# Kernel tuning notes

Hardware: AMD Instinct MI355X
Metric: run time of the kernel (lower is better)

The kernel has to match this reference:

```python
import jax, jax.numpy as jnp
import numpy as np

B, S, D, H = 1, 2048, 1024, 16
HD = D // H  # head_dim = 64
ROPE_BASE = 10000.0


def _rope_cos_sin(seqlen, head_dim, dtype):
    inv_freq = 1.0 / (ROPE_BASE ** (jnp.arange(0, head_dim, 2, dtype=jnp.float32) / head_dim))
    t = jnp.arange(seqlen, dtype=jnp.float32)
    freqs = jnp.outer(t, inv_freq)                      # [S, HD/2]
    emb = jnp.concatenate([freqs, freqs], axis=-1)      # [S, HD]
    # broadcast shape [1, S, 1, HD] over (batch, seq, heads, head_dim)
    return jnp.cos(emb)[None, :, None, :].astype(dtype), jnp.sin(emb)[None, :, None, :].astype(dtype)


def _rotate_half(x):
    x1, x2 = jnp.split(x, 2, axis=-1)
    return jnp.concatenate([-x2, x1], axis=-1)


def setup_inputs() -> dict:
    key = jax.random.key(0)
    k1, k2, k3 = jax.random.split(key, 3)
    std_in = 1.0 / np.sqrt(D)
    std_out = std_in / np.sqrt(2.0)  # layer_id = 0
    x = jax.random.normal(k1, (B, S, D), dtype=jnp.float32)
    w_in = jax.random.normal(k2, (3 * H * HD, D), dtype=jnp.float32) * std_in
    w_out = jax.random.normal(k3, (D, H * HD), dtype=jnp.float32) * std_out
    return {"x": x, "w_in": w_in, "w_out": w_out, "is_causal": 1}


def reference(x, w_in, w_out, is_causal):
    b, s, _ = x.shape
    qkv = jnp.einsum('bsd,ed->bse', x, w_in)            # [B,S,3*H*HD]
    xq, xk, xv = jnp.split(qkv, 3, axis=-1)
    xq = xq.reshape(b, s, H, HD)
    xk = xk.reshape(b, s, H, HD)
    xv = xv.reshape(b, s, H, HD)
    cos, sin = _rope_cos_sin(s, HD, xq.dtype)
    xq = xq * cos + _rotate_half(xq) * sin
    xk = xk * cos + _rotate_half(xk) * sin
    scale = 1.0 / np.sqrt(HD)
    scores = jnp.einsum('bqhd,bkhd->bhqk', xq, xk) * scale  # [B,H,S,S]
    if is_causal:
        mask = jnp.tril(jnp.ones((s, s), dtype=bool))
        scores = jnp.where(mask[None, None], scores, jnp.finfo(scores.dtype).min)
    probs = jax.nn.softmax(scores, axis=-1)
    out = jnp.einsum('bhqk,bkhd->bqhd', probs, xv)      # [B,S,H,HD]
    out = out.reshape(b, s, H * HD)
    return jnp.einsum('bse,de->bsd', out, w_out)
```

## Files before the change

kernel.cpp:

```cpp
#include <hip/hip_runtime.h>
#include <stdint.h>

#define S_LEN 2048
#define DMODEL 1024
#define NHEAD 16
#define HDIM 64
#define NE 3072
#define C2 0.18033688011112042f
#define RINV (-13.287712379549449f / 32.f)

typedef __attribute__((ext_vector_type(8))) short short8_t;
typedef __attribute__((ext_vector_type(4))) float f32x4;
typedef __attribute__((ext_vector_type(16))) float f32x16;

__device__ __forceinline__ float bf2f(ushort u) {
  union { float f; uint32_t i; } c; c.i = ((uint32_t)u) << 16; return c.f;
}
__device__ __forceinline__ ushort f2bf(float f) {
  union { float f; uint32_t i; } c; c.f = f;
  uint32_t x = c.i;
  return (ushort)((x + 0x7fffu + ((x >> 16) & 1u)) >> 16);
}

__device__ __forceinline__ void gload_lds16(const ushort* g, ushort* l) {
  __builtin_amdgcn_global_load_lds(
      (const __attribute__((address_space(1))) void*)g,
      (__attribute__((address_space(3))) void*)l, 16, 0, 0);
}

__global__ void cvt_all(const float* __restrict__ x, const float* __restrict__ w_in,
                        const float* __restrict__ w_out,
                        ushort* __restrict__ xbf, ushort* __restrict__ winbf,
                        ushort* __restrict__ woutbf) {
  int i = blockIdx.x * blockDim.x + threadIdx.x;
  const float* src; ushort* dst; int off;
  if (i < 524288)       { src = x;     dst = xbf;    off = i; }
  else if (i < 1310720) { src = w_in;  dst = winbf;  off = i - 524288; }
  else                  { src = w_out; dst = woutbf; off = i - 1310720; }
  float4 v = ((const float4*)src)[off];
  ushort4 o;
  o.x = f2bf(v.x); o.y = f2bf(v.y); o.z = f2bf(v.z); o.w = f2bf(v.w);
  ((ushort4*)dst)[off] = o;
}

template<int BM, int BN, int BK, int MODE>
__global__ __launch_bounds__(256) void gemm_abt(
    const ushort* __restrict__ A, const ushort* __restrict__ B,
    void* __restrict__ Cv, ushort* __restrict__ kfrag, ushort* __restrict__ vfrag,
    int M, int N, int K)
{
  constexpr int AR = BM / 32;
  constexpr int AC = BN / 32;
  constexpr int NB = BK / 8;
  constexpr int RPC = 512 / BK;
  constexpr int NCH = (BM + BN) / RPC;
  constexpr int PG = NCH / 4;
  constexpr int KK = BK / 32;
  __shared__ ushort lds[(BM + BN) * BK];

  const int nbn = N / BN;
  const int bid = blockIdx.x;
  int bm, bn;
  if constexpr (MODE == 2) {
    int xcd = bid & 7, local = bid >> 3;
    int cc = local / 24, ii = local % 24;
    bm = 2 * xcd + ii / 12;
    bn = cc * 12 + ii % 12;
  } else {
    const int cpx = gridDim.x >> 3;
    int swz = (bid & 7) * cpx + (bid >> 3);
    bm = swz / nbn;
    bn = swz - bm * nbn;
  }
  const int tid = threadIdx.x;
  const int w = tid >> 6, l = tid & 63;
  const int wm = w >> 1, wn = w & 1;
  const int fr = l & 15, fg = l >> 4;

  f32x4 acc[AR][AC];
#pragma unroll
  for (int r = 0; r < AR; ++r)
#pragma unroll
    for (int c = 0; c < AC; ++c) acc[r][c] = (f32x4){0.f, 0.f, 0.f, 0.f};

  const ushort* gsrc[PG];
  ushort* ldst[PG];
#pragma unroll
  for (int i = 0; i < PG; ++i) {
    int ch = w + 4 * i;
    int row = ch * RPC + l / NB;
    int cb = (l % NB) ^ (row & (NB - 1));
    if (row < BM)
      gsrc[i] = A + (size_t)(bm * BM + row) * K + cb * 8;
    else
      gsrc[i] = B + (size_t)(bn * BN + (row - BM)) * K + cb * 8;
    ldst[i] = &lds[ch * 512];
  }

  const int sw = fr & (NB - 1);
  const int rowa = wm * (BM / 2) + fr;
  const int rowb = wn * (BN / 2) + fr;

  for (int k0 = 0; k0 < K; k0 += BK) {
    __syncthreads();
#pragma unroll
    for (int i = 0; i < PG; ++i) gload_lds16(gsrc[i] + k0, ldst[i]);
    __syncthreads();

#pragma unroll
    for (int kk = 0; kk < KK; ++kk) {
      short8_t af[AR], bfr[AC];
#pragma unroll
      for (int r = 0; r < AR; ++r) {
        union { short8_t v; uint4 q; } u;
        u.q = *(const uint4*)&lds[(rowa + r * 16) * BK + ((fg + 4 * kk) ^ sw) * 8];
        af[r] = u.v;
      }
#pragma unroll
      for (int c = 0; c < AC; ++c) {
        union { short8_t v; uint4 q; } u;
        u.q = *(const uint4*)&lds[BM * BK + (rowb + c * 16) * BK + ((fg + 4 * kk) ^ sw) * 8];
        bfr[c] = u.v;
      }
      __builtin_amdgcn_s_setprio(1);
#pragma unroll
      for (int r = 0; r < AR; ++r)
#pragma unroll
        for (int c = 0; c < AC; ++c)
          acc[r][c] = __builtin_amdgcn_mfma_f32_16x16x32_bf16(af[r], bfr[c], acc[r][c], 0, 0, 0);
      __builtin_amdgcn_s_setprio(0);
    }
  }

  if constexpr (MODE == 0) {
    const int row0 = bm * BM + wm * (BM / 2) + fg * 4;
    const int col0 = bn * BN + wn * (BN / 2) + fr;
#pragma unroll
    for (int r = 0; r < AR; ++r)
#pragma unroll
      for (int c = 0; c < AC; ++c)
#pragma unroll
        for (int j = 0; j < 4; ++j)
          ((float*)Cv)[(size_t)(row0 + r * 16 + j) * N + col0 + c * 16] = acc[r][c][j];
  } else {
    const int cls = bn >> 4;
    const int h = bn & 15;
    if (cls == 0) {
      const int row0 = bm * BM + wm * (BM / 2) + fg * 4;
      const int colq = bn * 64 + wn * 32 + fr;
      ushort* qb = (ushort*)Cv;
#pragma unroll
      for (int r = 0; r < AR; ++r)
#pragma unroll
        for (int c = 0; c < AC; ++c)
#pragma unroll
          for (int j = 0; j < 4; ++j)
            qb[(size_t)(row0 + r * 16 + j) * 1024 + colq + c * 16] = f2bf(acc[r][c][j]);
    } else {
      __syncthreads();
      ushort* T = lds;
#pragma unroll
      for (int r = 0; r < AR; ++r)
#pragma unroll
        for (int c = 0; c < AC; ++c)
#pragma unroll
          for (int j = 0; j < 4; ++j) {
            int rl = wm * 64 + r * 16 + fg * 4 + j;
            int cl = wn * 32 + c * 16 + fr;
            T[rl * 72 + cl] = f2bf(acc[r][c][j]);
          }
      __syncthreads();

      if (cls == 1) {
        const int ii = tid & 31;
        const float invf = exp2f((float)ii * RINV);
#pragma unroll
        for (int kk = 0; kk < 16; ++kk) {
          int key = (tid >> 5) * 16 + kk;
          float sn, cs;
          sincosf((float)(bm * 128 + key) * invf, &sn, &cs);
          float x1 = bf2f(T[key * 72 + ii]), x2 = bf2f(T[key * 72 + ii + 32]);
          T[key * 72 + ii]      = f2bf(x1 * cs - x2 * sn);
          T[key * 72 + ii + 32] = f2bf(x2 * cs + x1 * sn);
        }
        __syncthreads();
#pragma unroll
        for (int it = 0; it < 4; ++it) {
          int idx = tid + 256 * it;
          int tt = idx >> 9, e = idx & 511;
          int c2 = e >> 6, l2 = e & 63, q2 = l2 & 31, hi2 = l2 >> 5;
          int kh = c2 >> 2, ks = c2 & 3;
          uint4 v = *(const uint4*)&T[(64 * tt + 32 * kh + q2) * 72 + 16 * ks + 8 * hi2];
          *(uint4*)(kfrag + (size_t)(h * 32 + bm * 2 + tt) * 4096 + e * 8) = v;
        }
      } else {
#pragma unroll
        for (int it = 0; it < 4; ++it) {
          int idx = tid + 256 * it;
          int tt = idx >> 9, e = idx & 511;
          int c2 = e >> 6, l2 = e & 63, q2 = l2 & 31, hi2 = l2 >> 5;
          int ks = c2 >> 1, dh = c2 & 1;
          ushort tmp[8];
#pragma unroll
          for (int jj = 0; jj < 8; ++jj)
            tmp[jj] = T[(64 * tt + 16 * ks + 8 * hi2 + jj) * 72 + 32 * dh + q2];
          *(uint4*)(vfrag + (size_t)(h * 32 + bm * 2 + tt) * 4096 + e * 8) = *(const uint4*)tmp;
        }
      }
    }
  }
}

__global__ __launch_bounds__(256) void attn_mfma(
    const ushort* __restrict__ qbuf, const ushort* __restrict__ kfrag,
    const ushort* __restrict__ vfrag, ushort* __restrict__ O,
    const int* __restrict__ icausal)
{
  __shared__ ushort obf[4][32][68];
  __shared__ float mdl[4][32];

  const int bid = blockIdx.x;
  const int h = (bid & 7) * 2 + ((bid >> 3) & 1);
  const int i = bid >> 4;
  const int g = i & 15, k = i >> 4;
  const int qt = (k == 0) ? g : (k == 1) ? (63 - g) : (k == 2) ? (31 - g) : (32 + g);

  const int causal = *icausal;
  const int nt = causal ? ((qt >> 1) + 1) : (S_LEN / 64);

  const int tid = threadIdx.x;
  const int w = tid >> 6, l = tid & 63;
  const int q = l & 31, hi = l >> 5;
  const int q0 = qt * 32;
  const int qa = q0 + q;
  const int t0 = w * nt / 4, t1 = (w + 1) * nt / 4;

  short8_t qf[4];
  {
    const ushort* qp = qbuf + (size_t)qa * 1024 + h * HDIM + 8 * hi;
#pragma unroll
    for (int ks = 0; ks < 4; ++ks) {
      union { short8_t v; uint4 u; } uu;
      uu.u = *(const uint4*)(qp + 16 * ks);
      qf[ks] = uu.v;
    }
    union { short8_t v; ushort u[8]; } a0, a1, b0, b1;
    a0.v = qf[0]; a1.v = qf[1]; b0.v = qf[2]; b1.v = qf[3];
#pragma unroll
    for (int j = 0; j < 8; ++j) {
      {
        float invf = exp2f((float)(8 * hi + j) * RINV);
        float sn, cs; sincosf((float)qa * invf, &sn, &cs);
        float x1 = bf2f(a0.u[j]), x2 = bf2f(b0.u[j]);
        a0.u[j] = f2bf((x1 * cs - x2 * sn) * C2);
        b0.u[j] = f2bf((x2 * cs + x1 * sn) * C2);
      }
      {
        float invf = exp2f((float)(16 + 8 * hi + j) * RINV);
        float sn, cs; sincosf((float)qa * invf, &sn, &cs);
        float x1 = bf2f(a1.u[j]), x2 = bf2f(b1.u[j]);
        a1.u[j] = f2bf((x1 * cs - x2 * sn) * C2);
        b1.u[j] = f2bf((x2 * cs + x1 * sn) * C2);
      }
    }
    qf[0] = a0.v; qf[1] = a1.v; qf[2] = b0.v; qf[3] = b1.v;
  }

  const ushort* kb = kfrag + (size_t)(h * 32 + t0) * 4096 + l * 8;
  const ushort* vb = vfrag + (size_t)(h * 32 + t0) * 4096 + l * 8;

  float den = 0.f;
  f32x16 oacc[2];
#pragma unroll
  for (int d = 0; d < 2; ++d)
#pragma unroll
    for (int r = 0; r < 16; ++r) oacc[d][r] = 0.f;

  if (t0 < t1) {
    uint4 kq[8];
#pragma unroll
    for (int ks = 0; ks < 4; ++ks)
#pragma unroll
      for (int kh = 0; kh < 2; ++kh)
        kq[ks * 2 + kh] = *(const uint4*)(kb + (kh * 4 + ks) * 512);
    kb += 4096;

    for (int t = t0; t < t1; ++t) {
      uint4 vq[8];
#pragma unroll
      for (int c = 0; c < 8; ++c)
        vq[c] = *(const uint4*)(vb + c * 512);
      vb += 4096;

      f32x16 sacc[2];
#pragma unroll
      for (int kh = 0; kh < 2; ++kh)
#pragma unroll
        for (int r = 0; r < 16; ++r) sacc[kh][r] = 0.f;
      __builtin_amdgcn_s_setprio(1);
#pragma unroll
      for (int ks = 0; ks < 4; ++ks)
#pragma unroll
        for (int kh = 0; kh < 2; ++kh) {
          union { short8_t v; uint4 u; } ku;
          ku.u = kq[ks * 2 + kh];
          sacc[kh] = __builtin_amdgcn_mfma_f32_32x32x16_bf16(ku.v, qf[ks], sacc[kh], 0, 0, 0);
        }
      __builtin_amdgcn_s_setprio(0);

      if (t + 1 < t1) {
#pragma unroll
        for (int ks = 0; ks < 4; ++ks)
#pragma unroll
          for (int kh = 0; kh < 2; ++kh)
            kq[ks * 2 + kh] = *(const uint4*)(kb + (kh * 4 + ks) * 512);
        kb += 4096;
      }

      if (causal && t == nt - 1) {
        const int k0 = t * 64;
#pragma unroll
        for (int kh = 0; kh < 2; ++kh)
#pragma unroll
          for (int r = 0; r < 16; ++r)
            if (k0 + 32 * kh + (r & 3) + 8 * (r >> 2) + 4 * hi > qa) sacc[kh][r] = -3e38f;
      }

      float p0 = 0.f, p1 = 0.f, p2 = 0.f, p3 = 0.f;
      short8_t pa[4];
#pragma unroll
      for (int ks = 0; ks < 4; ++ks) {
        const int blk = ks >> 1, kp = (ks & 1) * 8;
        float e0 = exp2f(sacc[blk][kp + 0]);
        float e1 = exp2f(sacc[blk][kp + 1]);
        float e2 = exp2f(sacc[blk][kp + 2]);
        float e3 = exp2f(sacc[blk][kp + 3]);
        float e4 = exp2f(sacc[blk][kp + 4]);
        float e5 = exp2f(sacc[blk][kp + 5]);
        float e6 = exp2f(sacc[blk][kp + 6]);
        float e7 = exp2f(sacc[blk][kp + 7]);
        p0 += e0 + e4; p1 += e1 + e5; p2 += e2 + e6; p3 += e3 + e7;
        uint wL0, wL1, wH0, wH1;
        asm("v_cvt_pk_bf16_f32 %0, %1, %2" : "=v"(wL0) : "v"(e0), "v"(e1));
        asm("v_cvt_pk_bf16_f32 %0, %1, %2" : "=v"(wL1) : "v"(e2), "v"(e3));
        asm("v_cvt_pk_bf16_f32 %0, %1, %2" : "=v"(wH0) : "v"(e4), "v"(e5));
        asm("v_cvt_pk_bf16_f32 %0, %1, %2" : "=v"(wH1) : "v"(e6), "v"(e7));
        uint s0 = hi ? wL0 : wH0, s1 = hi ? wL1 : wH1;
        uint r0 = __shfl_xor(s0, 32), r1 = __shfl_xor(s1, 32);
        union { short8_t v; uint u[4]; } pu;
        pu.u[0] = hi ? r0 : wL0;
        pu.u[1] = hi ? r1 : wL1;
        pu.u[2] = hi ? wH0 : r0;
        pu.u[3] = hi ? wH1 : r1;
        pa[ks] = pu.v;
      }
      float psum = (p0 + p1) + (p2 + p3);
      psum += __shfl_xor(psum, 32);
      den += psum;

      __builtin_amdgcn_s_setprio(1);
#pragma unroll
      for (int ks = 0; ks < 4; ++ks)
#pragma unroll
        for (int dh = 0; dh < 2; ++dh) {
          union { short8_t v; uint4 u; } vu;
          vu.u = vq[ks * 2 + dh];
          oacc[dh] = __builtin_amdgcn_mfma_f32_32x32x16_bf16(vu.v, pa[ks], oacc[dh], 0, 0, 0);
        }
      __builtin_amdgcn_s_setprio(0);
    }
  }

#pragma unroll
  for (int dh = 0; dh < 2; ++dh)
#pragma unroll
    for (int rq = 0; rq < 4; ++rq) {
      uint a0, a1;
      asm("v_cvt_pk_bf16_f32 %0, %1, %2" : "=v"(a0) : "v"(oacc[dh][4 * rq + 0]), "v"(oacc[dh][4 * rq + 1]));
      asm("v_cvt_pk_bf16_f32 %0, %1, %2" : "=v"(a1) : "v"(oacc[dh][4 * rq + 2]), "v"(oacc[dh][4 * rq + 3]));
      uint2 dd; dd.x = a0; dd.y = a1;
      *(uint2*)&obf[w][q][32 * dh + 8 * rq + 4 * hi] = dd;
    }
  if (hi == 0) mdl[w][q] = den;
  __syncthreads();

  {
    const int qq = tid >> 3, d8 = tid & 7;
    float dt = mdl[0][qq] + mdl[1][qq] + mdl[2][qq] + mdl[3][qq];
    float inv = 1.f / dt;
    uint4 a = *(const uint4*)&obf[0][qq][d8 * 8];
    uint4 b = *(const uint4*)&obf[1][qq][d8 * 8];
    uint4 c = *(const uint4*)&obf[2][qq][d8 * 8];
    uint4 d = *(const uint4*)&obf[3][qq][d8 * 8];
    const ushort* ap = (const ushort*)&a;
    const ushort* bp = (const ushort*)&b;
    const ushort* cp = (const ushort*)&c;
    const ushort* dp = (const ushort*)&d;
    ushort out8[8];
#pragma unroll
    for (int e = 0; e < 8; ++e) {
      float acc = (bf2f(ap[e]) + bf2f(bp[e])) + (bf2f(cp[e]) + bf2f(dp[e]));
      out8[e] = f2bf(acc * inv);
    }
    *(uint4*)(O + (size_t)(q0 + qq) * DMODEL + h * HDIM + d8 * 8) = *(const uint4*)out8;
  }
}

extern "C" void kernel_launch(void* const* d_in, const int* in_sizes, int n_in,
                              void* d_out, int out_size, void* d_ws, size_t ws_size,
                              hipStream_t stream) {
  const float* x     = (const float*)d_in[0];
  const float* w_in  = (const float*)d_in[1];
  const float* w_out = (const float*)d_in[2];
  const int* icausal = (const int*)d_in[3];

  char* ws = (char*)d_ws;
  ushort* xbf    = (ushort*)(ws);
  ushort* winbf  = (ushort*)(ws + 4194304);
  ushort* woutbf = (ushort*)(ws + 10485760);
  ushort* qbuf   = (ushort*)(ws + 12582912);
  ushort* kfrag  = (ushort*)(ws + 16777216);
  ushort* vfrag  = (ushort*)(ws + 20971520);
  ushort* obuf   = (ushort*)(ws + 25165824);

  cvt_all<<<6144, 256, 0, stream>>>(x, w_in, w_out, xbf, winbf, woutbf);

  gemm_abt<128, 64, 128, 2><<<16 * 48, 256, 0, stream>>>(xbf, winbf, (void*)qbuf, kfrag, vfrag, 2048, 3072, 1024);
  attn_mfma<<<1024, 256, 0, stream>>>(qbuf, kfrag, vfrag, obuf, icausal);
  gemm_abt<64, 64, 128, 0><<<32 * 16, 256, 0, stream>>>(obuf, woutbf, d_out, nullptr, nullptr, 2048, 1024, 1024);
}
```

Before: 72.74 us.

## Fuse fp32-to-bf16 conversion into GEMM tile loads and drop the conversion kernel

Removes the standalone kernel that converted x, w_in and w_out to bf16. The GEMMs now read fp32 operands directly, convert them in registers with packed bf16 conversion instructions, and store the result into the swizzled LDS tile. The bf16 attention output still uses the async global-to-LDS path. This removes a kernel launch and a full write-then-reread round trip of the converted data. In exchange, the GEMM inner loop fetches twice the bytes per operand, converts shared weight tiles redundantly in every block, and replaces async LDS loads with synchronous loads routed through registers.

```diff
diff --git a/kernel.cpp b/kernel.cpp
--- a/kernel.cpp
+++ b/kernel.cpp
@@ -28,24 +28,9 @@
       (__attribute__((address_space(3))) void*)l, 16, 0, 0);
 }
 
-__global__ void cvt_all(const float* __restrict__ x, const float* __restrict__ w_in,
-                        const float* __restrict__ w_out,
-                        ushort* __restrict__ xbf, ushort* __restrict__ winbf,
-                        ushort* __restrict__ woutbf) {
-  int i = blockIdx.x * blockDim.x + threadIdx.x;
-  const float* src; ushort* dst; int off;
-  if (i < 524288)       { src = x;     dst = xbf;    off = i; }
-  else if (i < 1310720) { src = w_in;  dst = winbf;  off = i - 524288; }
-  else                  { src = w_out; dst = woutbf; off = i - 1310720; }
-  float4 v = ((const float4*)src)[off];
-  ushort4 o;
-  o.x = f2bf(v.x); o.y = f2bf(v.y); o.z = f2bf(v.z); o.w = f2bf(v.w);
-  ((ushort4*)dst)[off] = o;
-}
-
 template<int BM, int BN, int BK, int MODE>
 __global__ __launch_bounds__(256) void gemm_abt(
-    const ushort* __restrict__ A, const ushort* __restrict__ B,
+    const void* __restrict__ Av, const float* __restrict__ Bf,
     void* __restrict__ Cv, ushort* __restrict__ kfrag, ushort* __restrict__ vfrag,
     int M, int N, int K)
 {
@@ -83,18 +68,30 @@
 #pragma unroll
     for (int c = 0; c < AC; ++c) acc[r][c] = (f32x4){0.f, 0.f, 0.f, 0.f};
 
-  const ushort* gsrc[PG];
-  ushort* ldst[PG];
-#pragma unroll
-  for (int i = 0; i < PG; ++i) {
-    int ch = w + 4 * i;
-    int row = ch * RPC + l / NB;
-    int cb = (l % NB) ^ (row & (NB - 1));
-    if (row < BM)
-      gsrc[i] = A + (size_t)(bm * BM + row) * K + cb * 8;
-    else
-      gsrc[i] = B + (size_t)(bn * BN + (row - BM)) * K + cb * 8;
-    ldst[i] = &lds[ch * 512];
+  const char* gp[PG];
+  ushort* ldp[PG];
+  bool ia[PG];
+  {
+    const int lrow = l / NB, cb = l % NB;
+#pragma unroll
+    for (int i = 0; i < PG; ++i) {
+      int ch = w + 4 * i;
+      int row = ch * RPC + lrow;
+      int scb = cb ^ (row & (NB - 1));
+      ia[i] = (ch * RPC) < BM;
+      if (ia[i]) {
+        if constexpr (MODE == 0) {
+          gp[i] = (const char*)((const ushort*)Av + (size_t)(bm * BM + row) * K + scb * 8);
+          ldp[i] = &lds[ch * 512];
+        } else {
+          gp[i] = (const char*)((const float*)Av + (size_t)(bm * BM + row) * K + cb * 8);
+          ldp[i] = &lds[ch * 512 + lrow * BK + scb * 8];
+        }
+      } else {
+        gp[i] = (const char*)(Bf + (size_t)(bn * BN + (row - BM)) * K + cb * 8);
+        ldp[i] = &lds[ch * 512 + lrow * BK + scb * 8];
+      }
+    }
   }
 
   const int sw = fr & (NB - 1);
@@ -104,7 +101,22 @@
   for (int k0 = 0; k0 < K; k0 += BK) {
     __syncthreads();
 #pragma unroll
-    for (int i = 0; i < PG; ++i) gload_lds16(gsrc[i] + k0, ldst[i]);
+    for (int i = 0; i < PG; ++i) {
+      if (MODE == 0 && ia[i]) {
+        gload_lds16((const ushort*)gp[i] + k0, ldp[i]);
+      } else {
+        const float* s = (const float*)gp[i] + k0;
+        float4 f0 = *(const float4*)s;
+        float4 f1 = *(const float4*)(s + 4);
+        uint u0, u1, u2, u3;
+        asm("v_cvt_pk_bf16_f32 %0, %1, %2" : "=v"(u0) : "v"(f0.x), "v"(f0.y));
+        asm("v_cvt_pk_bf16_f32 %0, %1, %2" : "=v"(u1) : "v"(f0.z), "v"(f0.w));
+        asm("v_cvt_pk_bf16_f32 %0, %1, %2" : "=v"(u2) : "v"(f1.x), "v"(f1.y));
+        asm("v_cvt_pk_bf16_f32 %0, %1, %2" : "=v"(u3) : "v"(f1.z), "v"(f1.w));
+        uint4 uu; uu.x = u0; uu.y = u1; uu.z = u2; uu.w = u3;
+        *(uint4*)ldp[i] = uu;
+      }
+    }
     __syncthreads();
 
 #pragma unroll
@@ -415,17 +427,14 @@
   const int* icausal = (const int*)d_in[3];
 
   char* ws = (char*)d_ws;
-  ushort* xbf    = (ushort*)(ws);
-  ushort* winbf  = (ushort*)(ws + 4194304);
-  ushort* woutbf = (ushort*)(ws + 10485760);
   ushort* qbuf   = (ushort*)(ws + 12582912);
   ushort* kfrag  = (ushort*)(ws + 16777216);
   ushort* vfrag  = (ushort*)(ws + 20971520);
   ushort* obuf   = (ushort*)(ws + 25165824);
 
-  cvt_all<<<6144, 256, 0, stream>>>(x, w_in, w_out, xbf, winbf, woutbf);
-
-  gemm_abt<128, 64, 128, 2><<<16 * 48, 256, 0, stream>>>(xbf, winbf, (void*)qbuf, kfrag, vfrag, 2048, 3072, 1024);
+  gemm_abt<128, 64, 128, 2><<<16 * 48, 256, 0, stream>>>(
+      (const void*)x, w_in, (void*)qbuf, kfrag, vfrag, 2048, 3072, 1024);
   attn_mfma<<<1024, 256, 0, stream>>>(qbuf, kfrag, vfrag, obuf, icausal);
-  gemm_abt<64, 64, 128, 0><<<32 * 16, 256, 0, stream>>>(obuf, woutbf, d_out, nullptr, nullptr, 2048, 1024, 1024);
-}
+  gemm_abt<64, 64, 128, 0><<<32 * 16, 256, 0, stream>>>(
+      (const void*)obuf, w_out, d_out, nullptr, nullptr, 2048, 1024, 1024);
+}
```

Measured after the change: 89.35 us. 1.23x slower.
